# Kernel tuning notes

Measured on AMD Instinct MI355X. Metric: run time of the kernel, lower is better.

The kernel has to match this reference:

```python
import jax, jax.numpy as jnp
import numpy as np
import math

# neuralef_loss_cfg constants
T = 10.0
K_FEAT = 32          # num_nearestn_feature
K_PIX = ((10, 2.0), (10, 0.1))  # (num_nearestn_pixel{1,2}, distance_weight)
PIX_W = 0.05         # pixelwise_weight
ALPHA = 1.0


def setup_inputs() -> dict:
    key = jax.random.key(0)
    k1, k2, k3 = jax.random.split(key, 3)
    highlevel_feature = jax.random.normal(k1, (8, 1024, 768), dtype=jnp.float32)
    Psi = jax.random.normal(k2, (8, 1024, 64), dtype=jnp.float32)
    im = jax.random.normal(k3, (8, 3, 32, 32), dtype=jnp.float32)
    return {"highlevel_feature": highlevel_feature, "Psi": Psi, "im": im}


def _build_gram(highlevel_feature, im):
    """Feature kNN graph + pixel kNN graphs -> degree-normalized gram matrix."""
    bs, n, d = highlevel_feature.shape
    M = bs * n
    # --- feature affinity: cosine sim, mutual-ish kNN sparsification ---
    X = highlevel_feature.reshape(M, d)
    X = X / jnp.linalg.norm(X, axis=-1, keepdims=True)
    A = X @ X.T                                   # [M, M]
    A = A.at[jnp.diag_indices(M)].set(-jnp.inf)
    A = jnp.maximum(A, 0.0)                       # clamp(min=0); diag -inf -> 0
    vals, idx = jax.lax.top_k(A, K_FEAT)          # [M, K]
    res = jnp.zeros_like(A).at[jnp.arange(M)[:, None], idx].set(vals)
    A = (res + res.T) * 0.5

    # --- pixel affinity: RGB + weighted xy coordinates, euclidean kNN ---
    im = (im + 1.0) / 2.0
    h, w = im.shape[2], im.shape[3]
    hw = h * w
    x_ = jnp.tile(jnp.linspace(0.0, 1.0, w), (h,))          # [hw]
    y_ = jnp.repeat(jnp.linspace(0.0, 1.0, h), w)           # [hw]
    imf = im.reshape(bs, 3, hw).transpose(0, 2, 1)          # [bs, hw, 3]
    row = jnp.arange(hw)
    A_p = jnp.zeros((bs, hw, hw), dtype=bool)
    for k, dw in K_PIX:
        if k == 0:
            continue
        coords = jnp.broadcast_to(jnp.stack([x_ * dw, y_ * dw], -1), (bs, hw, 2))
        im2 = jnp.concatenate([imf, coords], axis=-1)       # [bs, hw, 5]
        sq = jnp.sum(im2 * im2, axis=-1)                    # [bs, hw]
        d2 = sq[:, :, None] + sq[:, None, :] - 2.0 * jnp.einsum('bnd,bmd->bnm', im2, im2)
        euc = -jnp.sqrt(jnp.maximum(d2, 0.0))               # -cdist
        euc = euc.at[:, row, row].set(-jnp.inf)
        _, pidx = jax.lax.top_k(euc, k)                     # [bs, hw, k]
        r = jnp.zeros((bs, hw, hw), dtype=bool).at[
            jnp.arange(bs)[:, None, None], row[None, :, None], pidx].set(True)
        A_p = A_p | r | r.transpose(0, 2, 1)

    A2 = jax.scipy.linalg.block_diag(*[A_p[i].astype(jnp.float32) for i in range(bs)])

    D = jax.lax.rsqrt(A.sum(-1))
    gram = A * D[None, :] * D[:, None]
    D2 = jax.lax.rsqrt(A2.sum(-1))
    gram2 = A2 * D2[None, :] * D2[:, None]
    return gram + gram2 * PIX_W                             # [M, M]


def reference(highlevel_feature, Psi, im):
    Psi = Psi.reshape(-1, Psi.shape[-1]) * math.sqrt(T)     # [M, kdim]
    gram = _build_gram(highlevel_feature, im)
    gP = gram @ Psi                                         # [M, kdim]
    R = Psi.T @ gP
    R_hat = jax.lax.stop_gradient(Psi).T @ gP               # no_sg = False
    kdim = Psi.shape[1]
    loss = -jnp.trace(R) / kdim
    reg = jnp.sum(jnp.triu(R_hat ** 2, 1)) / kdim
    return (loss, reg * ALPHA)
```

## Files before the change

kernel.cpp:

```cpp
#include <hip/hip_runtime.h>
#include <hip/hip_bf16.h>
#include <math.h>

constexpr int MT  = 8192;
constexpr int DF  = 768;
constexpr int KD  = 64;
constexpr int HWP = 1024;
constexpr int KF  = 32;
constexpr int KP  = 10;
constexpr int RPB = 256;
constexpr int CAP   = 24;
constexpr int CANDQ = 512;
constexpr int NTILE = 2080;
#define SQT 3.16227766016837933f
#define PIXW 0.05f
#define THR_BITS 0x2C7Bu

typedef __bf16 bf16x8 __attribute__((ext_vector_type(8)));
typedef __bf16 bf16x4 __attribute__((ext_vector_type(4)));
typedef float  f32x4  __attribute__((ext_vector_type(4)));
typedef unsigned u32x4 __attribute__((ext_vector_type(4)));
typedef unsigned short u16x8 __attribute__((ext_vector_type(8)));
typedef _Float16 f16;

__device__ inline void tile_map(int bid, int& ti, int& tj) {
  const int xcd = bid & 7;
  const int s = bid >> 3;
  const int p = s / 65, r = s % 65;
  const int c1 = xcd * 4 + p;
  if (r <= c1) { ti = r; tj = c1; }
  else         { ti = r - c1 - 1; tj = 63 - c1; }
}
__device__ inline int tile_idx(int ti, int tj) {
  return ti * 64 - (ti * (ti - 1)) / 2 + (tj - ti);
}

__global__ __launch_bounds__(256) void prep_input_kernel(const float* __restrict__ X,
                                                         __bf16* __restrict__ Xb,
                                                         const float* __restrict__ im,
                                                         unsigned* __restrict__ pmask,
                                                         float* __restrict__ frow) {
  __shared__ float fr[HWP], fg[HWP], fb[HWP];
  __shared__ float red[256];
  const int tid = threadIdx.x;
  if (blockIdx.x < MT) {
    const int row = blockIdx.x;
    if (tid == 0) frow[row] = 0.f;
    const float4* xr4 = (const float4*)(X + (size_t)row * DF);
    float4 v = make_float4(0.f, 0.f, 0.f, 0.f);
    float s = 0.f;
    if (tid < 192) {
      v = xr4[tid];
      s = v.x * v.x + v.y * v.y + v.z * v.z + v.w * v.w;
    }
    red[tid] = s; __syncthreads();
    for (int o = 128; o > 0; o >>= 1) { if (tid < o) red[tid] += red[tid + o]; __syncthreads(); }
    const float rn = rsqrtf(red[0]);
    if (tid < 192) {
      bf16x4 o;
      o[0] = (__bf16)(v.x * rn); o[1] = (__bf16)(v.y * rn);
      o[2] = (__bf16)(v.z * rn); o[3] = (__bf16)(v.w * rn);
      *(bf16x4*)(Xb + (size_t)row * DF + tid * 4) = o;
    }
    return;
  }
  const int bx = blockIdx.x - MT;
  const int lane = tid & 63, wv = tid >> 6;
  const int b = bx >> 8;
  const int p = ((bx & 255) << 2) + wv;
  const float* imb = im + (size_t)b * 3 * HWP;
  for (int q = tid; q < HWP; q += 256) {
    fr[q] = imb[q]; fg[q] = imb[HWP + q]; fb[q] = imb[2 * HWP + q];
  }
  __syncthreads();
  const float pr = fr[p], pg = fg[p], pb = fb[p];
  const float px = (float)(p & 31) * (1.f / 31.f), py = (float)(p >> 5) * (1.f / 31.f);
  float d0[16], d1[16];
  #pragma unroll
  for (int i = 0; i < 16; ++i) {
    const int q = lane + (i << 6);
    float dr = (fr[q] - pr) * 0.5f, dg = (fg[q] - pg) * 0.5f, db = (fb[q] - pb) * 0.5f;
    float drgb = dr * dr + dg * dg + db * db;
    float dx = (float)(q & 31) * (1.f / 31.f) - px;
    float dy = (float)(q >> 5) * (1.f / 31.f) - py;
    float cd = dx * dx + dy * dy;
    d0[i] = (q == p) ? 1e30f : drgb + 4.00f * cd;
    d1[i] = (q == p) ? 1e30f : drgb + 0.01f * cd;
  }
  const int mrow = (b << 10) + p;
  auto doPass = [&](float (&dd)[16]) {
    for (int it = 0; it < KP; ++it) {
      float bm = 1e30f; int bq = 0;
      #pragma unroll
      for (int i = 0; i < 16; ++i) {
        const int q = lane + (i << 6);
        if (dd[i] < bm) { bm = dd[i]; bq = q; }
      }
      #pragma unroll
      for (int o = 32; o > 0; o >>= 1) {
        float ov = __shfl_down(bm, o);
        int   oq = __shfl_down(bq, o);
        if (ov < bm) { bm = ov; bq = oq; }
      }
      bq = __shfl(bq, 0);
      if (lane == 0) {
        atomicOr(&pmask[(size_t)mrow * 32 + (bq >> 5)], 1u << (bq & 31));
        atomicOr(&pmask[((size_t)((b << 10) + bq)) * 32 + (p >> 5)], 1u << (p & 31));
      }
      #pragma unroll
      for (int i = 0; i < 16; ++i)
        if (lane + (i << 6) == bq) dd[i] = 1e30f;
    }
  };
  doPass(d0);
  doPass(d1);
}

union SMem {
  struct { __bf16 A[128 * 64]; __bf16 B[128 * 64]; } st;
  f16 T[128 * 128];
};

__global__ __launch_bounds__(256) void gemm_kernel(const __bf16* __restrict__ Xb,
                                                   f16* __restrict__ Sp) {
  __shared__ SMem sm;
  const int tid = threadIdx.x;
  const int lane = tid & 63;
  const int wv = tid >> 6;
  const int wm = (wv & 1) * 64, wn = (wv >> 1) * 64;
  const int l15 = lane & 15, lq = lane >> 4;
  const int lr8 = lane >> 3, lc8 = lane & 7;
  const int rsw = l15 & 7;

  int ti, tj;
  tile_map(blockIdx.x, ti, tj);
  const int m0 = ti * 128;
  const int n0 = tj * 128;

  f32x4 acc[4][4];
  #pragma unroll
  for (int i = 0; i < 4; ++i)
    #pragma unroll
    for (int j = 0; j < 4; ++j)
      #pragma unroll
      for (int q = 0; q < 4; ++q) acc[i][j][q] = 0.f;

  for (int kt = 0; kt < 12; ++kt) {
    const int col0 = kt * 64;
    const __bf16* Ag = Xb + (size_t)m0 * DF + col0;
    const __bf16* Bg = Xb + (size_t)n0 * DF + col0;
    #pragma unroll
    for (int i = 0; i < 4; ++i) {
      const int r0 = (wv * 4 + i) * 8;
      const int csw = (lc8 ^ lr8) * 8;
      __builtin_amdgcn_global_load_lds(
          (const __attribute__((address_space(1))) void*)(Ag + (size_t)(r0 + lr8) * DF + csw),
          (__attribute__((address_space(3))) void*)(&sm.st.A[r0 * 64]), 16, 0, 0);
      __builtin_amdgcn_global_load_lds(
          (const __attribute__((address_space(1))) void*)(Bg + (size_t)(r0 + lr8) * DF + csw),
          (__attribute__((address_space(3))) void*)(&sm.st.B[r0 * 64]), 16, 0, 0);
    }
    __syncthreads();
    #pragma unroll
    for (int kk = 0; kk < 64; kk += 32) {
      bf16x8 af[4], bg[4];
      #pragma unroll
      for (int i = 0; i < 4; ++i)
        af[i] = *(const bf16x8*)(&sm.st.A[(wm + i * 16 + l15) * 64 + ((((kk >> 3) + lq) ^ rsw) * 8)]);
      #pragma unroll
      for (int j = 0; j < 4; ++j)
        bg[j] = *(const bf16x8*)(&sm.st.B[(wn + j * 16 + l15) * 64 + ((((kk >> 3) + lq) ^ rsw) * 8)]);
      #pragma unroll
      for (int i = 0; i < 4; ++i)
        #pragma unroll
        for (int j = 0; j < 4; ++j)
          acc[i][j] = __builtin_amdgcn_mfma_f32_16x16x32_bf16(af[i], bg[j], acc[i][j], 0, 0, 0);
    }
    __syncthreads();
  }
  #pragma unroll
  for (int i = 0; i < 4; ++i)
    #pragma unroll
    for (int j = 0; j < 4; ++j)
      #pragma unroll
      for (int q = 0; q < 4; ++q) {
        const int tr = wm + i * 16 + lq * 4 + q;
        const int tc = wn + j * 16 + l15;
        sm.T[tr * 128 + ((((tc >> 3) ^ (tr & 7)) << 3) | (tc & 7))] = (f16)acc[i][j][q];
      }
  __syncthreads();
  {
    f16* tile = Sp + (size_t)tile_idx(ti, tj) * (128 * 128);
    for (int e = tid; e < 128 * 16; e += 256) {
      const int r = e >> 4, ch = e & 15;
      const u32x4 v = *(const u32x4*)&sm.T[r * 128 + ((ch ^ (r & 7)) << 3)];
      __builtin_nontemporal_store(v, (u32x4*)&tile[r * 128 + ch * 8]);
    }
  }
}

constexpr int TS = 136;
__global__ __launch_bounds__(256) void compact_kernel(const f16* __restrict__ Sp,
                                                      unsigned* __restrict__ cnt2,
                                                      unsigned* __restrict__ cand) {
  __shared__ f16 T[128 * TS];
  const int tid = threadIdx.x;
  const int lane16 = tid & 15;
  int ti, tj;
  tile_map(blockIdx.x, ti, tj);
  const int m0 = ti * 128, n0 = tj * 128;
  const bool isdiag = (ti == tj);
  const f16* tile = Sp + (size_t)tile_idx(ti, tj) * (128 * 128);

  for (int e = tid; e < 128 * 16; e += 256) {
    const int rr = e >> 4, ch = e & 15;
    const u32x4 v = *(const u32x4*)&tile[(size_t)e * 8];
    *(u32x4*)&T[rr * TS + ch * 8] = v;
    const u16x8 vv = __builtin_bit_cast(u16x8, v);
    unsigned msk = 0;
    #pragma unroll
    for (int k = 0; k < 8; ++k) {
      const unsigned u = vv[k];
      if (u >= THR_BITS && u < 0x8000u) msk |= 1u << k;
    }
    if (isdiag) {
      const int kx = rr - ch * 8;
      if (kx >= 0 && kx < 8) msk &= ~(1u << kx);
    }
    const int cnt = __popc(msk);
    int x = cnt;
    #pragma unroll
    for (int o = 1; o < 16; o <<= 1) {
      const int y = __shfl_up(x, o);
      if (lane16 >= o) x += y;
    }
    const int gr = m0 + rr;
    int pos = x - cnt;
    const size_t slab = ((size_t)gr * 64 + tj) * CAP;
    unsigned m2 = msk;
    while (m2) {
      const int k = __ffs(m2) - 1; m2 &= m2 - 1;
      if (pos < CAP)
        __builtin_nontemporal_store(((unsigned)vv[k] << 16) | (unsigned)(8191 - (n0 + ch * 8 + k)),
                                    &cand[slab + pos]);
      ++pos;
    }
    if (lane16 == 15)
      __builtin_nontemporal_store((unsigned)min(x, CAP), &cnt2[(size_t)gr * 64 + tj]);
  }
  if (!isdiag) {
    __syncthreads();
    for (int e = tid; e < 128 * 16; e += 256) {
      const int rr = e >> 4, ch = e & 15;
      unsigned short us[8];
      unsigned msk = 0;
      #pragma unroll
      for (int k = 0; k < 8; ++k) {
        const int kk = (k + lane16) & 7;
        const unsigned u = __builtin_bit_cast(unsigned short, T[(ch * 8 + kk) * TS + rr]);
        us[kk] = (unsigned short)u;
        if (u >= THR_BITS && u < 0x8000u) msk |= 1u << kk;
      }
      const int cnt = __popc(msk);
      int x = cnt;
      #pragma unroll
      for (int o = 1; o < 16; o <<= 1) {
        const int y = __shfl_up(x, o);
        if (lane16 >= o) x += y;
      }
      const int gr = n0 + rr;
      int pos = x - cnt;
      const size_t slab = ((size_t)gr * 64 + ti) * CAP;
      unsigned m2 = msk;
      while (m2) {
        const int k = __ffs(m2) - 1; m2 &= m2 - 1;
        if (pos < CAP)
          __builtin_nontemporal_store(((unsigned)us[k] << 16) | (unsigned)(8191 - (m0 + ch * 8 + k)),
                                      &cand[slab + pos]);
        ++pos;
      }
      if (lane16 == 15)
        __builtin_nontemporal_store((unsigned)min(x, CAP), &cnt2[(size_t)gr * 64 + ti]);
    }
  }
}

__global__ __launch_bounds__(256) void select_kernel(const unsigned* __restrict__ cnt2,
                                                     const unsigned* __restrict__ cand,
                                                     int* __restrict__ fidx,
                                                     float* __restrict__ fval,
                                                     float* __restrict__ frow) {
  __shared__ unsigned cp[CANDQ];
  __shared__ int off[65];
  __shared__ float srow;
  const int tid = threadIdx.x;
  const int row = blockIdx.x;
  if (tid == 0) { off[0] = 0; srow = 0.f; }
  if (tid < 64) {
    int x = (int)cnt2[(size_t)row * 64 + tid];
    #pragma unroll
    for (int o = 1; o < 64; o <<= 1) {
      const int y = __shfl_up(x, o);
      if (tid >= o) x += y;
    }
    off[tid + 1] = x;
  }
  __syncthreads();
  const int n = min(off[64], CANDQ);
  {
    const int t = tid >> 2, k0 = tid & 3;
    const int o0 = off[t], ct = off[t + 1] - o0;
    const unsigned* slab = &cand[((size_t)row * 64 + t) * CAP];
    for (int k = k0; k < ct; k += 4)
      if (o0 + k < CANDQ) cp[o0 + k] = slab[k];
  }
  __syncthreads();
  for (int e = tid; e < n; e += 256) {
    const unsigned me = cp[e];
    int rank = 0;
    for (int j = 0; j < n; ++j) rank += (cp[j] > me);
    if (rank < KF) {
      union { unsigned short u; f16 h; } cvu; cvu.u = (unsigned short)(me >> 16);
      const float vv = (float)cvu.h;
      const int idx = 8191 - (int)(me & 0x1fffu);
      fval[(size_t)row * KF + rank] = vv;
      fidx[(size_t)row * KF + rank] = idx;
      atomicAdd(&frow[idx], 0.5f * vv);
      atomicAdd(&srow, 0.5f * vv);
    }
  }
  for (int rk = n + tid; rk < KF; rk += 256) {
    fval[(size_t)row * KF + rk] = 0.f;
    fidx[(size_t)row * KF + rk] = row;
  }
  __syncthreads();
  if (tid == 0) atomicAdd(&frow[row], srow);
}

__global__ void scales_kernel(const float* __restrict__ frow,
                              const unsigned* __restrict__ pmask,
                              float* __restrict__ sf, float* __restrict__ sp,
                              float* __restrict__ Rm) {
  int m = blockIdx.x * blockDim.x + threadIdx.x;
  if (m < KD * KD) Rm[m] = 0.f;
  if (m >= MT) return;
  const u32x4* pm = (const u32x4*)(pmask + (size_t)m * 32);
  int deg = 0;
  #pragma unroll
  for (int w = 0; w < 8; ++w) {
    const u32x4 bits = pm[w];
    deg += __popc(bits[0]) + __popc(bits[1]) + __popc(bits[2]) + __popc(bits[3]);
  }
  const float fr = frow[m];
  sf[m] = (fr > 0.f) ? rsqrtf(fr) * SQT : 0.f;
  sp[m] = (deg > 0) ? rsqrtf((float)deg) * SQT : 0.f;
}

__global__ __launch_bounds__(256) void gather_kernel(const int* __restrict__ fidx,
                                                     const float* __restrict__ fval,
                                                     const float* __restrict__ sf,
                                                     const float* __restrict__ sp,
                                                     const unsigned* __restrict__ pmask,
                                                     const float* __restrict__ Psi,
                                                     float* __restrict__ Wf,
                                                     float* __restrict__ W2) {
  __shared__ int list[4][64];
  __shared__ int cnts[4];
  const int w = threadIdx.x >> 6;
  const int t = threadIdx.x & 63;
  const int m = blockIdx.x * 4 + w;
  const int b = m >> 10;
  if (t == 0) cnts[w] = 0;
  __syncthreads();
  if (t < 32) {
    unsigned bits = pmask[(size_t)m * 32 + t];
    while (bits) {
      int bit = __ffs(bits) - 1;
      bits &= bits - 1;
      int pos = atomicAdd(&cnts[w], 1);
      if (pos < 64) list[w][pos] = t * 32 + bit;
    }
  }
  __syncthreads();
  float accf = 0.f;
  for (int k = 0; k < KF; ++k) {
    const float v = fval[m * KF + k];
    const int   c = fidx[m * KF + k];
    accf += 0.5f * v * sf[c] * Psi[(size_t)c * KD + t];
  }
  Wf[(size_t)m * KD + t] = accf;
  const int n = min(cnts[w], 64);
  float accp = 0.f;
  for (int e = 0; e < n; ++e) {
    const int g = b * HWP + list[w][e];
    accp += sp[g] * Psi[(size_t)g * KD + t];
  }
  W2[(size_t)m * KD + t] = accp;
}

__global__ __launch_bounds__(256) void rmat_part_kernel(const float* __restrict__ Psi,
                                                        const float* __restrict__ sf,
                                                        const float* __restrict__ sp,
                                                        const float* __restrict__ Wf,
                                                        const float* __restrict__ W2,
                                                        float* __restrict__ Pf,
                                                        float* __restrict__ Pp) {
  __shared__ float sPsi[8][KD], sWf[8][KD], sW2[8][KD];
  __shared__ float ssf[8], ssp[8];
  const int tid = threadIdx.x;
  const int c = tid & 63, g = tid >> 6;
  float accf[16], accp[16];
  #pragma unroll
  for (int i = 0; i < 16; ++i) { accf[i] = 0.f; accp[i] = 0.f; }
  const int rowBeg = blockIdx.x * (MT / RPB);
  for (int r0 = rowBeg; r0 < rowBeg + MT / RPB; r0 += 8) {
    #pragma unroll
    for (int e = tid; e < 8 * KD; e += 256) {
      const int r = e >> 6, cc = e & 63;
      const size_t gi = (size_t)(r0 + r) * KD + cc;
      sPsi[r][cc] = Psi[gi];
      sWf[r][cc]  = Wf[gi];
      sW2[r][cc]  = W2[gi];
    }
    if (tid < 8) { ssf[tid] = sf[r0 + tid]; ssp[tid] = sp[r0 + tid]; }
    __syncthreads();
    #pragma unroll
    for (int r = 0; r < 8; ++r) {
      const float wf = sWf[r][c], w2 = sW2[r][c];
      const float fsc = ssf[r], psc = ssp[r];
      const f32x4* p4 = (const f32x4*)&sPsi[r][g * 16];
      #pragma unroll
      for (int q = 0; q < 4; ++q) {
        const f32x4 pp = p4[q];
        #pragma unroll
        for (int k = 0; k < 4; ++k) {
          accf[q * 4 + k] += fsc * pp[k] * wf;
          accp[q * 4 + k] += psc * pp[k] * w2;
        }
      }
    }
    __syncthreads();
  }
  float* pf = Pf + (size_t)blockIdx.x * KD * KD;
  float* pp = Pp + (size_t)blockIdx.x * KD * KD;
  #pragma unroll
  for (int i = 0; i < 16; ++i) {
    const int a = g * 16 + i;
    pf[a * KD + c] = accf[i];
    pp[a * KD + c] = accp[i];
  }
}

__global__ __launch_bounds__(256) void rmat_reduce_kernel(const float* __restrict__ Pf,
                                                          const float* __restrict__ Pp,
                                                          float* __restrict__ Rm) {
  const int e = (blockIdx.x & 15) * 256 + threadIdx.x;
  const int grp = blockIdx.x >> 4;
  const int a = e >> 6, c = e & 63;
  const int eT = c * KD + a;
  float f = 0.f, ft = 0.f, p = 0.f;
  #pragma unroll 8
  for (int b = grp * 64; b < grp * 64 + 64; ++b) {
    f  += Pf[(size_t)b * KD * KD + e];
    ft += Pf[(size_t)b * KD * KD + eT];
    p  += Pp[(size_t)b * KD * KD + e];
  }
  atomicAdd(&Rm[e], f + ft + PIXW * p);
}

__global__ __launch_bounds__(256) void final_kernel(const float* __restrict__ Rm,
                                                    float* __restrict__ out) {
  __shared__ float redt[256], redr[256];
  const int tid = threadIdx.x;
  float tr = 0.f, rg = 0.f;
  for (int e = tid; e < KD * KD; e += 256) {
    int a = e >> 6, c = e & 63;
    float v = Rm[e];
    if (a == c) tr += v;
    else if (c > a) rg += v * v;
  }
  redt[tid] = tr; redr[tid] = rg;
  __syncthreads();
  for (int o = 128; o > 0; o >>= 1) {
    if (tid < o) { redt[tid] += redt[tid + o]; redr[tid] += redr[tid + o]; }
    __syncthreads();
  }
  if (tid == 0) {
    out[0] = -redt[0] / (float)KD;
    out[1] = redr[0] / (float)KD;
  }
}

extern "C" void kernel_launch(void* const* d_in, const int* in_sizes, int n_in,
                              void* d_out, int out_size, void* d_ws, size_t ws_size,
                              hipStream_t stream) {
  const float* hl  = (const float*)d_in[0];
  const float* Psi = (const float*)d_in[1];
  const float* im  = (const float*)d_in[2];
  float* out = (float*)d_out;

  char* ws = (char*)d_ws;
  size_t off = 0;
  auto alloc = [&](size_t bytes) -> void* {
    void* p = ws + off;
    off = (off + bytes + 255) & ~(size_t)255;
    return p;
  };
  f16*      Sp    = (f16*)alloc((size_t)NTILE * 128 * 128 * 2);
  unsigned* cand  = (unsigned*)alloc((size_t)MT * 64 * CAP * 4);
  unsigned* cnt2  = (unsigned*)alloc((size_t)MT * 64 * 4);
  __bf16*   Xb    = (__bf16*)alloc((size_t)MT * DF * 2);
  int*      fidx  = (int*)alloc((size_t)MT * KF * 4);
  float*    fval  = (float*)alloc((size_t)MT * KF * 4);
  float*    frow  = (float*)alloc((size_t)MT * 4);
  float*    sf    = (float*)alloc((size_t)MT * 4);
  float*    sp    = (float*)alloc((size_t)MT * 4);
  unsigned* pmask = (unsigned*)alloc((size_t)MT * 32 * 4);
  float*    Wf    = (float*)alloc((size_t)MT * KD * 4);
  float*    W2    = (float*)alloc((size_t)MT * KD * 4);
  float*    Pf    = (float*)alloc((size_t)RPB * KD * KD * 4);
  float*    Pp    = (float*)alloc((size_t)RPB * KD * KD * 4);
  float*    Rm    = (float*)alloc((size_t)KD * KD * 4);

  hipMemsetAsync(pmask, 0, (size_t)MT * 32 * 4, stream);

  prep_input_kernel<<<MT + MT / 4, 256, 0, stream>>>(hl, Xb, im, pmask, frow);
  gemm_kernel<<<NTILE, 256, 0, stream>>>(Xb, Sp);
  compact_kernel<<<NTILE, 256, 0, stream>>>(Sp, cnt2, cand);
  select_kernel<<<MT, 256, 0, stream>>>(cnt2, cand, fidx, fval, frow);
  scales_kernel<<<MT / 256, 256, 0, stream>>>(frow, pmask, sf, sp, Rm);
  gather_kernel<<<MT / 4, 256, 0, stream>>>(fidx, fval, sf, sp, pmask, Psi, Wf, W2);
  rmat_part_kernel<<<RPB, 256, 0, stream>>>(Psi, sf, sp, Wf, W2, Pf, Pp);
  rmat_reduce_kernel<<<64, 256, 0, stream>>>(Pf, Pp, Rm);
  final_kernel<<<1, 256, 0, stream>>>(Rm, out);
}
```

Before: 340.8 us.

## Write full symmetric similarity matrix and select candidates directly per row

The GEMM kernel now writes both the tile and its transpose into a full dense fp16 MxM similarity matrix, replacing packed triangular tiles. The separate compact kernel and its per-tile candidate slabs are removed. The select kernel instead scans each full row, counting and compacting above-threshold entries with wave ballots. This drops one kernel launch and the candidate-buffer round trip. In exchange, the GEMM writes twice as much data and the select kernel reads a 128 MB matrix, about 16 KB per row.

```diff
diff --git a/kernel.cpp b/kernel.cpp
--- a/kernel.cpp
+++ b/kernel.cpp
@@ -9,7 +9,6 @@
 constexpr int KF  = 32;
 constexpr int KP  = 10;
 constexpr int RPB = 256;
-constexpr int CAP   = 24;
 constexpr int CANDQ = 512;
 constexpr int NTILE = 2080;
 #define SQT 3.16227766016837933f
@@ -30,9 +29,6 @@
   const int c1 = xcd * 4 + p;
   if (r <= c1) { ti = r; tj = c1; }
   else         { ti = r - c1 - 1; tj = 63 - c1; }
-}
-__device__ inline int tile_idx(int ti, int tj) {
-  return ti * 64 - (ti * (ti - 1)) / 2 + (tj - ti);
 }
 
 __global__ __launch_bounds__(256) void prep_input_kernel(const float* __restrict__ X,
@@ -122,7 +118,7 @@
 };
 
 __global__ __launch_bounds__(256) void gemm_kernel(const __bf16* __restrict__ Xb,
-                                                   f16* __restrict__ Sp) {
+                                                   f16* __restrict__ S) {
   __shared__ SMem sm;
   const int tid = threadIdx.x;
   const int lane = tid & 63;
@@ -189,138 +185,89 @@
         sm.T[tr * 128 + ((((tc >> 3) ^ (tr & 7)) << 3) | (tc & 7))] = (f16)acc[i][j][q];
       }
   __syncthreads();
-  {
-    f16* tile = Sp + (size_t)tile_idx(ti, tj) * (128 * 128);
+  for (int e = tid; e < 128 * 16; e += 256) {
+    const int r = e >> 4, ch = e & 15;
+    const u32x4 v = *(const u32x4*)&sm.T[r * 128 + ((ch ^ (r & 7)) << 3)];
+    __builtin_nontemporal_store(v, (u32x4*)&S[(size_t)(m0 + r) * MT + n0 + ch * 8]);
+  }
+  if (m0 != n0) {
+    __syncthreads();
+    #pragma unroll
+    for (int i = 0; i < 4; ++i)
+      #pragma unroll
+      for (int j = 0; j < 4; ++j)
+        #pragma unroll
+        for (int q = 0; q < 4; ++q) {
+          const int tr = wm + i * 16 + lq * 4 + q;
+          const int tc = wn + j * 16 + l15;
+          sm.T[tc * 128 + ((((tr >> 3) ^ (tc & 7)) << 3) | (tr & 7))] = (f16)acc[i][j][q];
+        }
+    __syncthreads();
     for (int e = tid; e < 128 * 16; e += 256) {
       const int r = e >> 4, ch = e & 15;
       const u32x4 v = *(const u32x4*)&sm.T[r * 128 + ((ch ^ (r & 7)) << 3)];
-      __builtin_nontemporal_store(v, (u32x4*)&tile[r * 128 + ch * 8]);
-    }
-  }
-}
-
-constexpr int TS = 136;
-__global__ __launch_bounds__(256) void compact_kernel(const f16* __restrict__ Sp,
-                                                      unsigned* __restrict__ cnt2,
-                                                      unsigned* __restrict__ cand) {
-  __shared__ f16 T[128 * TS];
-  const int tid = threadIdx.x;
-  const int lane16 = tid & 15;
-  int ti, tj;
-  tile_map(blockIdx.x, ti, tj);
-  const int m0 = ti * 128, n0 = tj * 128;
-  const bool isdiag = (ti == tj);
-  const f16* tile = Sp + (size_t)tile_idx(ti, tj) * (128 * 128);
-
-  for (int e = tid; e < 128 * 16; e += 256) {
-    const int rr = e >> 4, ch = e & 15;
-    const u32x4 v = *(const u32x4*)&tile[(size_t)e * 8];
-    *(u32x4*)&T[rr * TS + ch * 8] = v;
-    const u16x8 vv = __builtin_bit_cast(u16x8, v);
-    unsigned msk = 0;
-    #pragma unroll
-    for (int k = 0; k < 8; ++k) {
-      const unsigned u = vv[k];
-      if (u >= THR_BITS && u < 0x8000u) msk |= 1u << k;
-    }
-    if (isdiag) {
-      const int kx = rr - ch * 8;
-      if (kx >= 0 && kx < 8) msk &= ~(1u << kx);
-    }
-    const int cnt = __popc(msk);
-    int x = cnt;
-    #pragma unroll
-    for (int o = 1; o < 16; o <<= 1) {
-      const int y = __shfl_up(x, o);
-      if (lane16 >= o) x += y;
-    }
-    const int gr = m0 + rr;
-    int pos = x - cnt;
-    const size_t slab = ((size_t)gr * 64 + tj) * CAP;
-    unsigned m2 = msk;
-    while (m2) {
-      const int k = __ffs(m2) - 1; m2 &= m2 - 1;
-      if (pos < CAP)
-        __builtin_nontemporal_store(((unsigned)vv[k] << 16) | (unsigned)(8191 - (n0 + ch * 8 + k)),
-                                    &cand[slab + pos]);
-      ++pos;
-    }
-    if (lane16 == 15)
-      __builtin_nontemporal_store((unsigned)min(x, CAP), &cnt2[(size_t)gr * 64 + tj]);
-  }
-  if (!isdiag) {
-    __syncthreads();
-    for (int e = tid; e < 128 * 16; e += 256) {
-      const int rr = e >> 4, ch = e & 15;
-      unsigned short us[8];
-      unsigned msk = 0;
-      #pragma unroll
-      for (int k = 0; k < 8; ++k) {
-        const int kk = (k + lane16) & 7;
-        const unsigned u = __builtin_bit_cast(unsigned short, T[(ch * 8 + kk) * TS + rr]);
-        us[kk] = (unsigned short)u;
-        if (u >= THR_BITS && u < 0x8000u) msk |= 1u << kk;
-      }
-      const int cnt = __popc(msk);
-      int x = cnt;
-      #pragma unroll
-      for (int o = 1; o < 16; o <<= 1) {
-        const int y = __shfl_up(x, o);
-        if (lane16 >= o) x += y;
-      }
-      const int gr = n0 + rr;
-      int pos = x - cnt;
-      const size_t slab = ((size_t)gr * 64 + ti) * CAP;
-      unsigned m2 = msk;
-      while (m2) {
-        const int k = __ffs(m2) - 1; m2 &= m2 - 1;
-        if (pos < CAP)
-          __builtin_nontemporal_store(((unsigned)us[k] << 16) | (unsigned)(8191 - (m0 + ch * 8 + k)),
-                                      &cand[slab + pos]);
-        ++pos;
-      }
-      if (lane16 == 15)
-        __builtin_nontemporal_store((unsigned)min(x, CAP), &cnt2[(size_t)gr * 64 + ti]);
-    }
-  }
-}
-
-__global__ __launch_bounds__(256) void select_kernel(const unsigned* __restrict__ cnt2,
-                                                     const unsigned* __restrict__ cand,
+      __builtin_nontemporal_store(v, (u32x4*)&S[(size_t)(n0 + r) * MT + m0 + ch * 8]);
+    }
+  }
+}
+
+__global__ __launch_bounds__(256) void select_kernel(const f16* __restrict__ S,
                                                      int* __restrict__ fidx,
                                                      float* __restrict__ fval,
                                                      float* __restrict__ frow) {
   __shared__ unsigned cp[CANDQ];
-  __shared__ int off[65];
+  __shared__ int wcnt[4];
   __shared__ float srow;
   const int tid = threadIdx.x;
   const int row = blockIdx.x;
-  if (tid == 0) { off[0] = 0; srow = 0.f; }
-  if (tid < 64) {
-    int x = (int)cnt2[(size_t)row * 64 + tid];
-    #pragma unroll
-    for (int o = 1; o < 64; o <<= 1) {
-      const int y = __shfl_up(x, o);
-      if (tid >= o) x += y;
-    }
-    off[tid + 1] = x;
-  }
-  __syncthreads();
-  const int n = min(off[64], CANDQ);
-  {
-    const int t = tid >> 2, k0 = tid & 3;
-    const int o0 = off[t], ct = off[t + 1] - o0;
-    const unsigned* slab = &cand[((size_t)row * 64 + t) * CAP];
-    for (int k = k0; k < ct; k += 4)
-      if (o0 + k < CANDQ) cp[o0 + k] = slab[k];
-  }
+  const int wv = tid >> 6, lane = tid & 63;
+  if (tid == 0) srow = 0.f;
+  const unsigned long long ltmask = (1ULL << lane) - 1ULL;
+  const u16x8* srow8 = (const u16x8*)(S + (size_t)row * MT);
+  u16x8 pk[4];
+  #pragma unroll
+  for (int i = 0; i < 4; ++i) pk[i] = srow8[i * 256 + tid];
+  unsigned tot = 0;
+  #pragma unroll
+  for (int i = 0; i < 4; ++i)
+    #pragma unroll
+    for (int j = 0; j < 8; ++j) {
+      const unsigned u = pk[i][j];
+      const int c = i * 2048 + tid * 8 + j;
+      const unsigned long long bal = __ballot(u >= THR_BITS && u < 0x8000u && c != row);
+      tot += (unsigned)__popcll(bal);
+    }
+  if (lane == 0) wcnt[wv] = (int)tot;
+  __syncthreads();
+  int base = 0, ntot = 0;
+  #pragma unroll
+  for (int w = 0; w < 4; ++w) {
+    if (w < wv) base += wcnt[w];
+    ntot += wcnt[w];
+  }
+  const int n = min(ntot, CANDQ);
+  int run = base;
+  #pragma unroll
+  for (int i = 0; i < 4; ++i)
+    #pragma unroll
+    for (int j = 0; j < 8; ++j) {
+      const unsigned u = pk[i][j];
+      const int c = i * 2048 + tid * 8 + j;
+      const bool pred = (u >= THR_BITS && u < 0x8000u && c != row);
+      const unsigned long long bal = __ballot(pred);
+      if (pred) {
+        const int pos = run + (int)__popcll(bal & ltmask);
+        if (pos < CANDQ) cp[pos] = (u << 16) | (unsigned)(8191 - c);
+      }
+      run += (int)__popcll(bal);
+    }
   __syncthreads();
   for (int e = tid; e < n; e += 256) {
     const unsigned me = cp[e];
     int rank = 0;
     for (int j = 0; j < n; ++j) rank += (cp[j] > me);
     if (rank < KF) {
-      union { unsigned short u; f16 h; } cvu; cvu.u = (unsigned short)(me >> 16);
+      union { unsigned short us; f16 h; } cvu; cvu.us = (unsigned short)(me >> 16);
       const float vv = (float)cvu.h;
       const int idx = 8191 - (int)(me & 0x1fffu);
       fval[(size_t)row * KF + rank] = vv;
@@ -506,9 +453,7 @@
     off = (off + bytes + 255) & ~(size_t)255;
     return p;
   };
-  f16*      Sp    = (f16*)alloc((size_t)NTILE * 128 * 128 * 2);
-  unsigned* cand  = (unsigned*)alloc((size_t)MT * 64 * CAP * 4);
-  unsigned* cnt2  = (unsigned*)alloc((size_t)MT * 64 * 4);
+  f16*      S     = (f16*)alloc((size_t)MT * MT * 2);
   __bf16*   Xb    = (__bf16*)alloc((size_t)MT * DF * 2);
   int*      fidx  = (int*)alloc((size_t)MT * KF * 4);
   float*    fval  = (float*)alloc((size_t)MT * KF * 4);
@@ -525,9 +470,8 @@
   hipMemsetAsync(pmask, 0, (size_t)MT * 32 * 4, stream);
 
   prep_input_kernel<<<MT + MT / 4, 256, 0, stream>>>(hl, Xb, im, pmask, frow);
-  gemm_kernel<<<NTILE, 256, 0, stream>>>(Xb, Sp);
-  compact_kernel<<<NTILE, 256, 0, stream>>>(Sp, cnt2, cand);
-  select_kernel<<<MT, 256, 0, stream>>>(cnt2, cand, fidx, fval, frow);
+  gemm_kernel<<<NTILE, 256, 0, stream>>>(Xb, S);
+  select_kernel<<<MT, 256, 0, stream>>>(S, fidx, fval, frow);
   scales_kernel<<<MT / 256, 256, 0, stream>>>(frow, pmask, sf, sp, Rm);
   gather_kernel<<<MT / 4, 256, 0, stream>>>(fidx, fval, sf, sp, pmask, Psi, Wf, W2);
   rmat_part_kernel<<<RPB, 256, 0, stream>>>(Psi, sf, sp, Wf, W2, Pf, Pp);
```

After: 318.7 us. 6.5% less time.
